# Kernel tuning notes

Measured on AMD Instinct MI355X. Metric: run time of the kernel, lower is better.

Reference implementation:

```python
import jax, jax.numpy as jnp
import numpy as np

N = 50000      # nodes per graph
E = 1600000    # edges per graph
D_IN = 128
D_HID = 128
D_OUT = 128
D_GF = 128
N_LAYERS = 3   # input->hid, hid->hid (hidden_layer=1), hid->out


def setup_inputs() -> dict:
    key = jax.random.key(0)
    ks = jax.random.split(key, 24)
    inp = {
        "feat_p": jax.random.normal(ks[0], (N, D_IN), jnp.float32),
        "src_p": jax.random.randint(ks[1], (E,), 0, N, jnp.int32),
        "dst_p": jax.random.randint(ks[2], (E,), 0, N, jnp.int32),
        "feat_s": jax.random.normal(ks[3], (N, D_IN), jnp.float32),
        "src_s": jax.random.randint(ks[4], (E,), 0, N, jnp.int32),
        "dst_s": jax.random.randint(ks[5], (E,), 0, N, jnp.int32),
    }
    dims = [(D_IN, D_HID), (D_HID, D_HID), (D_HID, D_OUT)]
    for i, (di, do) in enumerate(dims):
        inp[f"W{i}"] = jax.random.normal(ks[6 + 2 * i], (di, do), jnp.float32) * 0.05
        inp[f"b{i}"] = jnp.zeros((do,), jnp.float32)
    inp["Wr"] = jax.random.normal(ks[14], (D_OUT, D_GF), jnp.float32) * 0.05
    inp["br"] = jnp.zeros((D_GF,), jnp.float32)
    inp["Wm1"] = jax.random.normal(ks[15], (2 * D_GF, D_GF), jnp.float32) * 0.05
    inp["bm1"] = jnp.zeros((D_GF,), jnp.float32)
    inp["Wm2"] = jax.random.normal(ks[16], (D_GF, 1), jnp.float32) * 0.05
    inp["bm2"] = jnp.zeros((1,), jnp.float32)
    return inp


def _gcn_stack(feat, src, dst, layers):
    """Stacked GCN: mean over incoming messages, then linear.
    NOTE: the original SingleGCN never applies its ReLU (bug preserved)."""
    n = feat.shape[0]
    deg = jax.ops.segment_sum(jnp.ones_like(src, feat.dtype), dst, num_segments=n)
    inv_deg = (1.0 / jnp.maximum(deg, 1.0))[:, None]  # [N,1]
    h = feat
    for W, b in layers:
        msg = h[src]                                           # [E,d] gather
        agg = jax.ops.segment_sum(msg, dst, num_segments=n)    # [N,d] scatter-add
        h = (agg * inv_deg) @ W + b                            # mean + linear
    return h


def reference(feat_p, src_p, dst_p, feat_s, src_s, dst_s,
              W0, b0, W1, b1, W2, b2, Wr, br, Wm1, bm1, Wm2, bm2):
    layers = [(W0, b0), (W1, b1), (W2, b2)]
    h_p = _gcn_stack(feat_p, src_p, dst_p, layers)
    h_s = _gcn_stack(feat_s, src_s, dst_s, layers)
    # ReadOut: mean over nodes -> linear -> sigmoid
    g_p = jax.nn.sigmoid(jnp.mean(h_p, axis=0) @ Wr + br)  # [D_GF]
    g_s = jax.nn.sigmoid(jnp.mean(h_s, axis=0) @ Wr + br)
    # Match: concat -> linear -> linear -> sigmoid
    c = jnp.concatenate([g_p, g_s], axis=-1)               # [2*D_GF]
    d = (c @ Wm1 + bm1) @ Wm2 + bm2                        # [1]
    return jax.nn.sigmoid(d)
```

## Files before the change

### kernel.cpp

```cpp
#include <hip/hip_runtime.h>
#include <math.h>

#define D 128
#define BSH 9
#define NPB 512
#define BCAP 17920
#define STCAP 6252


__global__ __launch_bounds__(256) void zero_kernel(float* __restrict__ buf, int n4) {
    float4* b4 = (float4*)buf;
    const float4 z = make_float4(0.f, 0.f, 0.f, 0.f);
    const int stride = gridDim.x * 256;
    for (int i = blockIdx.x * 256 + threadIdx.x; i < n4; i += stride) b4[i] = z;
}

__global__ __launch_bounds__(512) void bin_kernel(
        const int* __restrict__ src_p, const int* __restrict__ dst_p,
        const int* __restrict__ src_s, const int* __restrict__ dst_s,
        int* __restrict__ sbins, unsigned short* __restrict__ dbins,
        unsigned* __restrict__ cur, int E, int nbkt) {
    const int g = blockIdx.y;
    const int* src = g ? src_s : src_p;
    const int* dst = g ? dst_s : dst_p;
    int* sb = sbins + (size_t)g * nbkt * BCAP;
    unsigned short* db = dbins + (size_t)g * nbkt * BCAP;
    unsigned* scur = cur + g * nbkt;
    unsigned* dcur = cur + 2 * nbkt + g * nbkt;

    __shared__ int sstage[STCAP];
    __shared__ unsigned short dstage[STCAP];
    __shared__ unsigned hist_s[128], hist_d[128];
    __shared__ unsigned offs_s[128], offs_d[128];
    __shared__ unsigned lcur_s[128], lcur_d[128];
    __shared__ unsigned gb_s[128], gb_d[128];

    const int tid = threadIdx.x;
    const int wv = tid >> 6, lane = tid & 63;
    for (int i = tid; i < 128; i += 512) { hist_s[i] = 0u; hist_d[i] = 0u; }
    __syncthreads();

    const int e0 = blockIdx.x * STCAP;
    const int e1 = min(e0 + STCAP, E);
    const int efull = e0 + ((e1 - e0) & ~3);

    for (int e = e0 + tid * 4; e + 4 <= e1; e += 512 * 4) {
        int4 s4 = *(const int4*)(src + e);
        int4 d4 = *(const int4*)(dst + e);
        atomicAdd(&hist_s[s4.x >> BSH], 1u);
        atomicAdd(&hist_s[s4.y >> BSH], 1u);
        atomicAdd(&hist_s[s4.z >> BSH], 1u);
        atomicAdd(&hist_s[s4.w >> BSH], 1u);
        atomicAdd(&hist_d[d4.x >> BSH], 1u);
        atomicAdd(&hist_d[d4.y >> BSH], 1u);
        atomicAdd(&hist_d[d4.z >> BSH], 1u);
        atomicAdd(&hist_d[d4.w >> BSH], 1u);
    }
    for (int e = efull + tid; e < e1; e += 512) {
        atomicAdd(&hist_s[src[e] >> BSH], 1u);
        atomicAdd(&hist_d[dst[e] >> BSH], 1u);
    }
    __syncthreads();

    if (wv == 0 || wv == 1) {
        const unsigned* h = (wv == 0) ? hist_s : hist_d;
        unsigned* o = (wv == 0) ? offs_s : offs_d;
        unsigned* lc = (wv == 0) ? lcur_s : lcur_d;
        unsigned a = (2 * lane < nbkt) ? h[2 * lane] : 0u;
        unsigned b = (2 * lane + 1 < nbkt) ? h[2 * lane + 1] : 0u;
        unsigned v = a + b;
        for (int d2 = 1; d2 < 64; d2 <<= 1) {
            unsigned t = __shfl_up(v, d2);
            if (lane >= d2) v += t;
        }
        unsigned ex = v - (a + b);
        if (2 * lane < nbkt) { o[2 * lane] = ex; lc[2 * lane] = ex; }
        if (2 * lane + 1 < nbkt) { o[2 * lane + 1] = ex + a; lc[2 * lane + 1] = ex + a; }
    } else if (wv == 2) {
        for (int i = lane; i < nbkt; i += 64) {
            unsigned c = hist_s[i];
            gb_s[i] = c ? atomicAdd(&scur[i], c) : 0u;
        }
    } else if (wv == 3) {
        for (int i = lane; i < nbkt; i += 64) {
            unsigned c = hist_d[i];
            gb_d[i] = c ? atomicAdd(&dcur[i], c) : 0u;
        }
    }
    __syncthreads();

    for (int e = e0 + tid * 4; e + 4 <= e1; e += 512 * 4) {
        int4 s4 = *(const int4*)(src + e);
        int4 d4 = *(const int4*)(dst + e);
        int sv[4] = {s4.x, s4.y, s4.z, s4.w};
        int dv[4] = {d4.x, d4.y, d4.z, d4.w};
        #pragma unroll
        for (int k = 0; k < 4; ++k) {
            unsigned p = atomicAdd(&lcur_s[sv[k] >> BSH], 1u);
            sstage[p] = ((sv[k] & (NPB - 1)) << 17) | dv[k];
            unsigned pd = atomicAdd(&lcur_d[dv[k] >> BSH], 1u);
            dstage[pd] = (unsigned short)(dv[k] & (NPB - 1));
        }
    }
    for (int e = efull + tid; e < e1; e += 512) {
        int s = src[e], d2 = dst[e];
        unsigned p = atomicAdd(&lcur_s[s >> BSH], 1u);
        sstage[p] = ((s & (NPB - 1)) << 17) | d2;
        unsigned pd = atomicAdd(&lcur_d[d2 >> BSH], 1u);
        dstage[pd] = (unsigned short)(d2 & (NPB - 1));
    }
    __syncthreads();

    for (int b = wv; b < nbkt; b += 8) {
        unsigned cs = hist_s[b], os = offs_s[b], gs = gb_s[b];
        unsigned lim = (gs < (unsigned)BCAP) ? min(cs, (unsigned)BCAP - gs) : 0u;
        int* dp = sb + (size_t)b * BCAP + gs;
        for (unsigned i = lane; i < lim; i += 64) dp[i] = sstage[os + i];
        unsigned cd = hist_d[b], od = offs_d[b], gd = gb_d[b];
        unsigned limd = (gd < (unsigned)BCAP) ? min(cd, (unsigned)BCAP - gd) : 0u;
        unsigned short* ddp = db + (size_t)b * BCAP + gd;
        for (unsigned i = lane; i < limd; i += 64) ddp[i] = dstage[od + i];
    }
}

__global__ __launch_bounds__(512) void deg_inv(
        const unsigned short* __restrict__ dbins, const unsigned* __restrict__ cur,
        float* __restrict__ inv, int N, int nbkt) {
    const int q = blockIdx.x, g = blockIdx.y;
    const unsigned short* bin = dbins + (size_t)(g * nbkt + q) * BCAP;
    const int cnt = min((int)cur[2 * nbkt + g * nbkt + q], BCAP);
    const int tid = threadIdx.x;
    const int wv = tid >> 6;
    __shared__ float bl[8][NPB];
    for (int i = tid; i < 8 * NPB; i += 512) ((float*)bl)[i] = 0.f;
    __syncthreads();
    float* mybl = bl[wv];
    const ushort4* b4 = (const ushort4*)bin;
    const int n4 = cnt >> 2;
    for (int i = tid; i < n4; i += 512) {
        ushort4 v = b4[i];
        atomicAdd(&mybl[v.x], 1.f);
        atomicAdd(&mybl[v.y], 1.f);
        atomicAdd(&mybl[v.z], 1.f);
        atomicAdd(&mybl[v.w], 1.f);
    }
    for (int e = (n4 << 2) + tid; e < cnt; e += 512) atomicAdd(&mybl[bin[e]], 1.f);
    __syncthreads();
    float t = 0.f;
    #pragma unroll
    for (int r = 0; r < 8; ++r) t += bl[r][tid];
    int node = q * NPB + tid;
    if (node < N) inv[(size_t)g * N + node] = 1.0f / fmaxf(t, 1.0f);
}

__global__ __launch_bounds__(512) void prop_scan(
        const int* __restrict__ sbins, const unsigned* __restrict__ cur,
        const float* __restrict__ w, const float* __restrict__ inv,
        float* __restrict__ out_w, float* __restrict__ out_u,
        float* __restrict__ sums, int s_idx, int N, int nbkt, float scale) {
    const int q = blockIdx.x, g = blockIdx.y;
    const int* bin = sbins + (size_t)(g * nbkt + q) * BCAP;
    const int cnt = min((int)cur[g * nbkt + q], BCAP);
    const float* wg = w + (size_t)g * N;
    const int tid = threadIdx.x;
    const int wv = tid >> 6;
    __shared__ float bl[8][NPB];
    __shared__ float red[512];
    for (int i = tid; i < 8 * NPB; i += 512) ((float*)bl)[i] = 0.f;
    __syncthreads();
    float* mybl = bl[wv];
    const int4* b4 = (const int4*)bin;
    const int n4 = cnt >> 2;
    for (int i = tid; i < n4; i += 512) {
        int4 v = b4[i];
        float a = wg[v.x & 0x1FFFF];
        float b = wg[v.y & 0x1FFFF];
        float c = wg[v.z & 0x1FFFF];
        float d2 = wg[v.w & 0x1FFFF];
        atomicAdd(&mybl[((unsigned)v.x) >> 17], a);
        atomicAdd(&mybl[((unsigned)v.y) >> 17], b);
        atomicAdd(&mybl[((unsigned)v.z) >> 17], c);
        atomicAdd(&mybl[((unsigned)v.w) >> 17], d2);
    }
    for (int e = (n4 << 2) + tid; e < cnt; e += 512) {
        int v = bin[e];
        atomicAdd(&mybl[((unsigned)v) >> 17], wg[v & 0x1FFFF]);
    }
    __syncthreads();
    float t = 0.f;
    #pragma unroll
    for (int r = 0; r < 8; ++r) t += bl[r][tid];
    const float u = t * scale;
    const int node = q * NPB + tid;
    const bool valid = node < N;
    if (valid) {
        size_t off = (size_t)g * N + node;
        if (out_w) out_w[off] = u * inv[off];
        if (out_u) out_u[off] = u;
    }
    if (sums) {
        red[tid] = valid ? u : 0.f;
        __syncthreads();
        for (int st = 256; st > 0; st >>= 1) {
            if (tid < st) red[tid] += red[tid + st];
            __syncthreads();
        }
        if (tid == 0 && red[0] != 0.f) atomicAdd(&sums[g * 2 + s_idx], red[0]);
    }
}

__global__ __launch_bounds__(256) void featsum_kernel(
        const float* __restrict__ feat_p, const float* __restrict__ feat_s,
        const float* __restrict__ u3, float* __restrict__ fpart2,
        int N, int rpb) {
    const int g = blockIdx.y;
    const float* feat = g ? feat_s : feat_p;
    const float* u = u3 + (size_t)g * N;
    const int col4 = threadIdx.x & 31;
    const int rgrp = threadIdx.x >> 5;
    const int r0 = blockIdx.x * rpb;
    const int r1 = min(r0 + rpb, N);

    const float4* f4 = (const float4*)feat;
    float4 acc = make_float4(0.f, 0.f, 0.f, 0.f);
    for (int n = r0 + rgrp * 4; n + 3 < r1; n += 32) {
        float4 uu = *(const float4*)(u + n);
        float4 v0 = f4[(size_t)n * 32 + col4];
        float4 v1 = f4[(size_t)(n + 1) * 32 + col4];
        float4 v2 = f4[(size_t)(n + 2) * 32 + col4];
        float4 v3 = f4[(size_t)(n + 3) * 32 + col4];
        acc.x += uu.x * v0.x + uu.y * v1.x + uu.z * v2.x + uu.w * v3.x;
        acc.y += uu.x * v0.y + uu.y * v1.y + uu.z * v2.y + uu.w * v3.y;
        acc.z += uu.x * v0.z + uu.y * v1.z + uu.z * v2.z + uu.w * v3.z;
        acc.w += uu.x * v0.w + uu.y * v1.w + uu.z * v2.w + uu.w * v3.w;
    }
    __shared__ float4 smem[256];
    smem[threadIdx.x] = acc;
    __syncthreads();
    if (rgrp == 0) {
        float4 t = smem[col4];
        #pragma unroll
        for (int k = 1; k < 8; k++) {
            float4 o = smem[k * 32 + col4];
            t.x += o.x; t.y += o.y; t.z += o.z; t.w += o.w;
        }
        float* dst = fpart2 + ((size_t)g * 16 + (blockIdx.x & 15)) * 128 + col4 * 4;
        atomicAdd(dst + 0, t.x);
        atomicAdd(dst + 1, t.y);
        atomicAdd(dst + 2, t.z);
        atomicAdd(dst + 3, t.w);
    }
}

__global__ __launch_bounds__(512) void final_kernel(
        const float* __restrict__ fpart2,
        const float* __restrict__ sums,
        const float* __restrict__ W0, const float* __restrict__ b0,
        const float* __restrict__ W1, const float* __restrict__ b1,
        const float* __restrict__ W2, const float* __restrict__ b2,
        const float* __restrict__ Wr, const float* __restrict__ br,
        const float* __restrict__ Wm1, const float* __restrict__ bm1,
        const float* __restrict__ Wm2, const float* __restrict__ bm2,
        float* __restrict__ out) {
    __shared__ float x[128];
    __shared__ float part[4][128];
    __shared__ float rvec[256];
    __shared__ float Avec[128], Bvec[128];
    __shared__ float gv[256];
    const int tid = threadIdx.x;
    const int j = tid & 127;
    const int h = tid >> 7;

    auto mv128 = [&](const float* __restrict__ W, float* __restrict__ buf) {
        float p = 0.f;
        const float* Wp = W + (size_t)(h * 32) * 128 + j;
        #pragma unroll
        for (int i = 0; i < 32; ++i) p += buf[h * 32 + i] * Wp[(size_t)i * 128];
        part[h][j] = p;
        __syncthreads();
        if (h == 0) buf[j] = part[0][j] + part[1][j] + part[2][j] + part[3][j];
        __syncthreads();
    };

    if (tid < 256) {
        int g = tid >> 7;
        const float* fp = fpart2 + (size_t)g * 2048 + (tid & 127);
        float rv = 0.f;
        #pragma unroll
        for (int b = 0; b < 16; ++b) rv += fp[(size_t)b * 128];
        rvec[tid] = rv;
    }
    __syncthreads();

    if (tid < 128) x[tid] = b0[tid];
    __syncthreads();
    mv128(W1, x);
    mv128(W2, x);
    if (tid < 128) Avec[tid] = x[tid];
    __syncthreads();
    if (tid < 128) x[tid] = b1[tid];
    __syncthreads();
    mv128(W2, x);
    if (tid < 128) Bvec[tid] = x[tid];
    __syncthreads();

    for (int g = 0; g < 2; ++g) {
        const float s1 = sums[g * 2 + 0];
        const float s2 = sums[g * 2 + 1];
        if (tid < 128) x[tid] = rvec[g * 128 + tid];
        __syncthreads();
        mv128(W0, x);
        mv128(W1, x);
        mv128(W2, x);
        if (tid < 128) x[tid] += s2 * Avec[tid] + s1 * Bvec[tid] + b2[tid];
        __syncthreads();
        mv128(Wr, x);
        if (tid < 128) gv[g * 128 + tid] = 1.0f / (1.0f + expf(-(x[tid] + br[tid])));
        __syncthreads();
    }

    {
        float p = 0.f;
        const float* Wp = Wm1 + (size_t)(h * 64) * 128 + j;
        #pragma unroll
        for (int i = 0; i < 64; ++i) p += gv[h * 64 + i] * Wp[(size_t)i * 128];
        part[h][j] = p;
        __syncthreads();
        if (h == 0)
            part[0][j] = (part[0][j] + part[1][j] + part[2][j] + part[3][j] + bm1[j]) * Wm2[j];
        __syncthreads();
        if (tid < 64) part[0][tid] += part[0][tid + 64];
        __syncthreads();
        if (tid < 32) part[0][tid] += part[0][tid + 32];
        __syncthreads();
        if (tid < 16) part[0][tid] += part[0][tid + 16];
        __syncthreads();
        if (tid < 8) part[0][tid] += part[0][tid + 8];
        __syncthreads();
        if (tid < 4) part[0][tid] += part[0][tid + 4];
        __syncthreads();
        if (tid < 2) part[0][tid] += part[0][tid + 2];
        __syncthreads();
        if (tid == 0) out[0] = 1.0f / (1.0f + expf(-(part[0][0] + part[0][1] + bm2[0])));
    }
}

extern "C" void kernel_launch(void* const* d_in, const int* in_sizes, int n_in,
                              void* d_out, int out_size, void* d_ws, size_t ws_size,
                              hipStream_t stream) {
    const float* feat_p = (const float*)d_in[0];
    const int*   src_p  = (const int*)d_in[1];
    const int*   dst_p  = (const int*)d_in[2];
    const float* feat_s = (const float*)d_in[3];
    const int*   src_s  = (const int*)d_in[4];
    const int*   dst_s  = (const int*)d_in[5];
    const float* W0 = (const float*)d_in[6];
    const float* b0 = (const float*)d_in[7];
    const float* W1 = (const float*)d_in[8];
    const float* b1 = (const float*)d_in[9];
    const float* W2 = (const float*)d_in[10];
    const float* b2 = (const float*)d_in[11];
    const float* Wr = (const float*)d_in[12];
    const float* br = (const float*)d_in[13];
    const float* Wm1 = (const float*)d_in[14];
    const float* bm1 = (const float*)d_in[15];
    const float* Wm2 = (const float*)d_in[16];
    const float* bm2 = (const float*)d_in[17];
    float* out = (float*)d_out;

    const int N = in_sizes[0] / D;
    const int E = in_sizes[1];
    const int N2 = 2 * N;
    const int nbkt = (N + NPB - 1) >> BSH;
    const int NBB = (E + STCAP - 1) / STCAP;
    const int FB = 256;
    const int rpb = (((N + FB - 1) / FB) + 3) & ~3;

    float* ws       = (float*)d_ws;
    unsigned* cur   = (unsigned*)ws;
    const int curN  = (4 * nbkt + 3) & ~3;
    float* sums     = ws + curN;
    float* fpart2   = sums + 16;
    float* inv      = fpart2 + 2 * 16 * 128;
    float* w1       = inv + N2;
    float* w2       = w1 + N2;
    float* u3       = w2 + N2;
    int*   sbins    = (int*)(u3 + N2);
    unsigned short* dbins = (unsigned short*)(sbins + (size_t)2 * nbkt * BCAP);

    const float u0 = 1.0f / (float)N;
    const int zc4 = (curN + 16 + 2 * 16 * 128) / 4;

    zero_kernel<<<16, 256, 0, stream>>>(ws, zc4);

    bin_kernel<<<dim3(NBB, 2), 512, 0, stream>>>(src_p, dst_p, src_s, dst_s,
                                                 sbins, dbins, cur, E, nbkt);

    deg_inv<<<dim3(nbkt, 2), 512, 0, stream>>>(dbins, cur, inv, N, nbkt);

    prop_scan<<<dim3(nbkt, 2), 512, 0, stream>>>(sbins, cur, inv, inv,
                                                 w1, nullptr, sums, 0,
                                                 N, nbkt, u0);
    prop_scan<<<dim3(nbkt, 2), 512, 0, stream>>>(sbins, cur, w1, inv,
                                                 w2, nullptr, sums, 1,
                                                 N, nbkt, 1.0f);
    prop_scan<<<dim3(nbkt, 2), 512, 0, stream>>>(sbins, cur, w2, inv,
                                                 nullptr, u3, nullptr, 0,
                                                 N, nbkt, 1.0f);

    featsum_kernel<<<dim3(FB, 2), 256, 0, stream>>>(feat_p, feat_s, u3, fpart2, N, rpb);

    final_kernel<<<1, 512, 0, stream>>>(fpart2, sums, W0, b0, W1, b1, W2, b2,
                                        Wr, br, Wm1, bm1, Wm2, bm2, out);
}
```

Measured before the change: 279.4 us.

## Use fixed per-block bin slots, drop global atomics, fuse featsum into last propagation

The binning kernel now writes each edge block's bucket contents into a fixed-size per-(bucket, block) slot with a count array. This replaces global atomic cursors into shared bins, so the zero kernel goes away and the workspace is instead cleared inside deg_inv. The feature-weighted node sum is folded into the final propagation pass, which removes the separate featsum kernel and the u3 buffer. In exchange, readers now scan padded slots with per-element bounds checks. Any block-bucket holding more than 128 edges is silently truncated, and the zeroing inside deg_inv must finish before the later kernels read sums and fpart2.

```diff
diff --git a/kernel.cpp b/kernel.cpp
--- a/kernel.cpp
+++ b/kernel.cpp
@@ -4,43 +4,38 @@
 #define D 128
 #define BSH 9
 #define NPB 512
-#define BCAP 17920
+#define SLOT 128
 #define STCAP 6252
-
-
-__global__ __launch_bounds__(256) void zero_kernel(float* __restrict__ buf, int n4) {
-    float4* b4 = (float4*)buf;
-    const float4 z = make_float4(0.f, 0.f, 0.f, 0.f);
-    const int stride = gridDim.x * 256;
-    for (int i = blockIdx.x * 256 + threadIdx.x; i < n4; i += stride) b4[i] = z;
-}
+#define NBB 256
+#define NBKT_MAX 128
+
 
 __global__ __launch_bounds__(512) void bin_kernel(
         const int* __restrict__ src_p, const int* __restrict__ dst_p,
         const int* __restrict__ src_s, const int* __restrict__ dst_s,
         int* __restrict__ sbins, unsigned short* __restrict__ dbins,
-        unsigned* __restrict__ cur, int E, int nbkt) {
-    const int g = blockIdx.y;
+        unsigned* __restrict__ cnt_s, unsigned* __restrict__ cnt_d,
+        int E, int nbkt) {
+    const int g = blockIdx.y, b = blockIdx.x;
     const int* src = g ? src_s : src_p;
     const int* dst = g ? dst_s : dst_p;
-    int* sb = sbins + (size_t)g * nbkt * BCAP;
-    unsigned short* db = dbins + (size_t)g * nbkt * BCAP;
-    unsigned* scur = cur + g * nbkt;
-    unsigned* dcur = cur + 2 * nbkt + g * nbkt;
+    int* sb = sbins + (size_t)g * nbkt * NBB * SLOT;
+    unsigned short* db = dbins + (size_t)g * nbkt * NBB * SLOT;
+    unsigned* csp = cnt_s + (size_t)g * nbkt * NBB;
+    unsigned* cdp = cnt_d + (size_t)g * nbkt * NBB;
 
     __shared__ int sstage[STCAP];
     __shared__ unsigned short dstage[STCAP];
-    __shared__ unsigned hist_s[128], hist_d[128];
-    __shared__ unsigned offs_s[128], offs_d[128];
-    __shared__ unsigned lcur_s[128], lcur_d[128];
-    __shared__ unsigned gb_s[128], gb_d[128];
+    __shared__ unsigned hist_s[NBKT_MAX], hist_d[NBKT_MAX];
+    __shared__ unsigned offs_s[NBKT_MAX], offs_d[NBKT_MAX];
+    __shared__ unsigned lcur_s[NBKT_MAX], lcur_d[NBKT_MAX];
 
     const int tid = threadIdx.x;
     const int wv = tid >> 6, lane = tid & 63;
-    for (int i = tid; i < 128; i += 512) { hist_s[i] = 0u; hist_d[i] = 0u; }
-    __syncthreads();
-
-    const int e0 = blockIdx.x * STCAP;
+    for (int i = tid; i < NBKT_MAX; i += 512) { hist_s[i] = 0u; hist_d[i] = 0u; }
+    __syncthreads();
+
+    const int e0 = b * STCAP;
     const int e1 = min(e0 + STCAP, E);
     const int efull = e0 + ((e1 - e0) & ~3);
 
@@ -67,25 +62,15 @@
         unsigned* o = (wv == 0) ? offs_s : offs_d;
         unsigned* lc = (wv == 0) ? lcur_s : lcur_d;
         unsigned a = (2 * lane < nbkt) ? h[2 * lane] : 0u;
-        unsigned b = (2 * lane + 1 < nbkt) ? h[2 * lane + 1] : 0u;
-        unsigned v = a + b;
+        unsigned bb = (2 * lane + 1 < nbkt) ? h[2 * lane + 1] : 0u;
+        unsigned v = a + bb;
         for (int d2 = 1; d2 < 64; d2 <<= 1) {
             unsigned t = __shfl_up(v, d2);
             if (lane >= d2) v += t;
         }
-        unsigned ex = v - (a + b);
+        unsigned ex = v - (a + bb);
         if (2 * lane < nbkt) { o[2 * lane] = ex; lc[2 * lane] = ex; }
         if (2 * lane + 1 < nbkt) { o[2 * lane + 1] = ex + a; lc[2 * lane + 1] = ex + a; }
-    } else if (wv == 2) {
-        for (int i = lane; i < nbkt; i += 64) {
-            unsigned c = hist_s[i];
-            gb_s[i] = c ? atomicAdd(&scur[i], c) : 0u;
-        }
-    } else if (wv == 3) {
-        for (int i = lane; i < nbkt; i += 64) {
-            unsigned c = hist_d[i];
-            gb_d[i] = c ? atomicAdd(&dcur[i], c) : 0u;
-        }
     }
     __syncthreads();
 
@@ -111,40 +96,45 @@
     }
     __syncthreads();
 
-    for (int b = wv; b < nbkt; b += 8) {
-        unsigned cs = hist_s[b], os = offs_s[b], gs = gb_s[b];
-        unsigned lim = (gs < (unsigned)BCAP) ? min(cs, (unsigned)BCAP - gs) : 0u;
-        int* dp = sb + (size_t)b * BCAP + gs;
-        for (unsigned i = lane; i < lim; i += 64) dp[i] = sstage[os + i];
-        unsigned cd = hist_d[b], od = offs_d[b], gd = gb_d[b];
-        unsigned limd = (gd < (unsigned)BCAP) ? min(cd, (unsigned)BCAP - gd) : 0u;
-        unsigned short* ddp = db + (size_t)b * BCAP + gd;
-        for (unsigned i = lane; i < limd; i += 64) ddp[i] = dstage[od + i];
+    for (int q = wv; q < nbkt; q += 8) {
+        unsigned cs = min(hist_s[q], (unsigned)SLOT);
+        unsigned os = offs_s[q];
+        int* dp = sb + ((size_t)q * NBB + b) * SLOT;
+        for (unsigned i = lane; i < cs; i += 64) dp[i] = sstage[os + i];
+        unsigned cd = min(hist_d[q], (unsigned)SLOT);
+        unsigned od = offs_d[q];
+        unsigned short* ddp = db + ((size_t)q * NBB + b) * SLOT;
+        for (unsigned i = lane; i < cd; i += 64) ddp[i] = dstage[od + i];
+        if (lane == 0) { csp[q * NBB + b] = cs; cdp[q * NBB + b] = cd; }
     }
 }
 
 __global__ __launch_bounds__(512) void deg_inv(
-        const unsigned short* __restrict__ dbins, const unsigned* __restrict__ cur,
-        float* __restrict__ inv, int N, int nbkt) {
+        const unsigned short* __restrict__ dbins, const unsigned* __restrict__ cnt_d,
+        float* __restrict__ inv, float* __restrict__ zbase, int zcount,
+        int N, int nbkt) {
     const int q = blockIdx.x, g = blockIdx.y;
-    const unsigned short* bin = dbins + (size_t)(g * nbkt + q) * BCAP;
-    const int cnt = min((int)cur[2 * nbkt + g * nbkt + q], BCAP);
-    const int tid = threadIdx.x;
-    const int wv = tid >> 6;
+    const int tid = threadIdx.x, wv = tid >> 6;
+    if (q == 0 && g == 0)
+        for (int i = tid; i < zcount; i += 512) zbase[i] = 0.f;
+    const unsigned short* dq = dbins + ((size_t)g * nbkt + q) * NBB * SLOT;
+    const unsigned* cq = cnt_d + (size_t)g * nbkt * NBB + (size_t)q * NBB;
     __shared__ float bl[8][NPB];
+    __shared__ unsigned lcnt[NBB];
+    if (tid < NBB) lcnt[tid] = cq[tid];
     for (int i = tid; i < 8 * NPB; i += 512) ((float*)bl)[i] = 0.f;
     __syncthreads();
     float* mybl = bl[wv];
-    const ushort4* b4 = (const ushort4*)bin;
-    const int n4 = cnt >> 2;
-    for (int i = tid; i < n4; i += 512) {
-        ushort4 v = b4[i];
+    const ushort4* d4 = (const ushort4*)dq;
+    for (int i = tid; i < NBB * (SLOT / 4); i += 512) {
+        int lim = (int)lcnt[i >> 5] - ((i & 31) << 2);
+        if (lim <= 0) continue;
+        ushort4 v = d4[i];
         atomicAdd(&mybl[v.x], 1.f);
-        atomicAdd(&mybl[v.y], 1.f);
-        atomicAdd(&mybl[v.z], 1.f);
-        atomicAdd(&mybl[v.w], 1.f);
-    }
-    for (int e = (n4 << 2) + tid; e < cnt; e += 512) atomicAdd(&mybl[bin[e]], 1.f);
+        if (lim > 1) atomicAdd(&mybl[v.y], 1.f);
+        if (lim > 2) atomicAdd(&mybl[v.z], 1.f);
+        if (lim > 3) atomicAdd(&mybl[v.w], 1.f);
+    }
     __syncthreads();
     float t = 0.f;
     #pragma unroll
@@ -154,37 +144,40 @@
 }
 
 __global__ __launch_bounds__(512) void prop_scan(
-        const int* __restrict__ sbins, const unsigned* __restrict__ cur,
+        const int* __restrict__ sbins, const unsigned* __restrict__ cnt_s,
         const float* __restrict__ w, const float* __restrict__ inv,
-        float* __restrict__ out_w, float* __restrict__ out_u,
-        float* __restrict__ sums, int s_idx, int N, int nbkt, float scale) {
+        float* __restrict__ out_w,
+        const float* __restrict__ feat_p, const float* __restrict__ feat_s,
+        float* __restrict__ fpart2, float* __restrict__ sums, int s_idx,
+        int N, int nbkt, float scale) {
     const int q = blockIdx.x, g = blockIdx.y;
-    const int* bin = sbins + (size_t)(g * nbkt + q) * BCAP;
-    const int cnt = min((int)cur[g * nbkt + q], BCAP);
+    const int* sq = sbins + ((size_t)g * nbkt + q) * NBB * SLOT;
+    const unsigned* cq = cnt_s + (size_t)g * nbkt * NBB + (size_t)q * NBB;
     const float* wg = w + (size_t)g * N;
-    const int tid = threadIdx.x;
-    const int wv = tid >> 6;
+    const int tid = threadIdx.x, wv = tid >> 6;
     __shared__ float bl[8][NPB];
-    __shared__ float red[512];
+    __shared__ unsigned lcnt[NBB];
+    __shared__ float red[NPB];
+    if (tid < NBB) lcnt[tid] = cq[tid];
     for (int i = tid; i < 8 * NPB; i += 512) ((float*)bl)[i] = 0.f;
     __syncthreads();
     float* mybl = bl[wv];
-    const int4* b4 = (const int4*)bin;
-    const int n4 = cnt >> 2;
-    for (int i = tid; i < n4; i += 512) {
-        int4 v = b4[i];
+    const int4* s4 = (const int4*)sq;
+    for (int i = tid; i < NBB * (SLOT / 4); i += 512) {
+        int lim = (int)lcnt[i >> 5] - ((i & 31) << 2);
+        if (lim <= 0) continue;
+        int4 v = s4[i];
+        int iy = (lim > 1) ? (v.y & 0x1FFFF) : 0;
+        int iz = (lim > 2) ? (v.z & 0x1FFFF) : 0;
+        int iw = (lim > 3) ? (v.w & 0x1FFFF) : 0;
         float a = wg[v.x & 0x1FFFF];
-        float b = wg[v.y & 0x1FFFF];
-        float c = wg[v.z & 0x1FFFF];
-        float d2 = wg[v.w & 0x1FFFF];
+        float b2 = wg[iy];
+        float c2 = wg[iz];
+        float d2 = wg[iw];
         atomicAdd(&mybl[((unsigned)v.x) >> 17], a);
-        atomicAdd(&mybl[((unsigned)v.y) >> 17], b);
-        atomicAdd(&mybl[((unsigned)v.z) >> 17], c);
-        atomicAdd(&mybl[((unsigned)v.w) >> 17], d2);
-    }
-    for (int e = (n4 << 2) + tid; e < cnt; e += 512) {
-        int v = bin[e];
-        atomicAdd(&mybl[((unsigned)v) >> 17], wg[v & 0x1FFFF]);
+        if (lim > 1) atomicAdd(&mybl[((unsigned)v.y) >> 17], b2);
+        if (lim > 2) atomicAdd(&mybl[((unsigned)v.z) >> 17], c2);
+        if (lim > 3) atomicAdd(&mybl[((unsigned)v.w) >> 17], d2);
     }
     __syncthreads();
     float t = 0.f;
@@ -193,10 +186,9 @@
     const float u = t * scale;
     const int node = q * NPB + tid;
     const bool valid = node < N;
-    if (valid) {
+    if (valid && out_w) {
         size_t off = (size_t)g * N + node;
-        if (out_w) out_w[off] = u * inv[off];
-        if (out_u) out_u[off] = u;
+        out_w[off] = u * inv[off];
     }
     if (sums) {
         red[tid] = valid ? u : 0.f;
@@ -207,48 +199,24 @@
         }
         if (tid == 0 && red[0] != 0.f) atomicAdd(&sums[g * 2 + s_idx], red[0]);
     }
-}
-
-__global__ __launch_bounds__(256) void featsum_kernel(
-        const float* __restrict__ feat_p, const float* __restrict__ feat_s,
-        const float* __restrict__ u3, float* __restrict__ fpart2,
-        int N, int rpb) {
-    const int g = blockIdx.y;
-    const float* feat = g ? feat_s : feat_p;
-    const float* u = u3 + (size_t)g * N;
-    const int col4 = threadIdx.x & 31;
-    const int rgrp = threadIdx.x >> 5;
-    const int r0 = blockIdx.x * rpb;
-    const int r1 = min(r0 + rpb, N);
-
-    const float4* f4 = (const float4*)feat;
-    float4 acc = make_float4(0.f, 0.f, 0.f, 0.f);
-    for (int n = r0 + rgrp * 4; n + 3 < r1; n += 32) {
-        float4 uu = *(const float4*)(u + n);
-        float4 v0 = f4[(size_t)n * 32 + col4];
-        float4 v1 = f4[(size_t)(n + 1) * 32 + col4];
-        float4 v2 = f4[(size_t)(n + 2) * 32 + col4];
-        float4 v3 = f4[(size_t)(n + 3) * 32 + col4];
-        acc.x += uu.x * v0.x + uu.y * v1.x + uu.z * v2.x + uu.w * v3.x;
-        acc.y += uu.x * v0.y + uu.y * v1.y + uu.z * v2.y + uu.w * v3.y;
-        acc.z += uu.x * v0.z + uu.y * v1.z + uu.z * v2.z + uu.w * v3.z;
-        acc.w += uu.x * v0.w + uu.y * v1.w + uu.z * v2.w + uu.w * v3.w;
-    }
-    __shared__ float4 smem[256];
-    smem[threadIdx.x] = acc;
-    __syncthreads();
-    if (rgrp == 0) {
-        float4 t = smem[col4];
-        #pragma unroll
-        for (int k = 1; k < 8; k++) {
-            float4 o = smem[k * 32 + col4];
-            t.x += o.x; t.y += o.y; t.z += o.z; t.w += o.w;
+    if (fpart2) {
+        red[tid] = valid ? u : 0.f;
+        __syncthreads();
+        const float* feat = g ? feat_s : feat_p;
+        const int j = tid & 127, rg = tid >> 7;
+        const int base = q * NPB;
+        const int rmax = min(NPB, N - base);
+        float acc = 0.f;
+        const int rend = min((rg + 1) * 128, rmax);
+        for (int r = rg * 128; r < rend; ++r)
+            acc += red[r] * feat[(size_t)(base + r) * D + j];
+        ((float*)bl)[rg * 128 + j] = acc;
+        __syncthreads();
+        if (rg == 0) {
+            float tot = ((float*)bl)[j] + ((float*)bl)[128 + j] +
+                        ((float*)bl)[256 + j] + ((float*)bl)[384 + j];
+            atomicAdd(&fpart2[((size_t)g * 16 + (q & 15)) * D + j], tot);
         }
-        float* dst = fpart2 + ((size_t)g * 16 + (blockIdx.x & 15)) * 128 + col4 * 4;
-        atomicAdd(dst + 0, t.x);
-        atomicAdd(dst + 1, t.y);
-        atomicAdd(dst + 2, t.z);
-        atomicAdd(dst + 3, t.w);
     }
 }
 
@@ -372,43 +340,37 @@
     const int E = in_sizes[1];
     const int N2 = 2 * N;
     const int nbkt = (N + NPB - 1) >> BSH;
-    const int NBB = (E + STCAP - 1) / STCAP;
-    const int FB = 256;
-    const int rpb = (((N + FB - 1) / FB) + 3) & ~3;
-
-    float* ws       = (float*)d_ws;
-    unsigned* cur   = (unsigned*)ws;
-    const int curN  = (4 * nbkt + 3) & ~3;
-    float* sums     = ws + curN;
-    float* fpart2   = sums + 16;
-    float* inv      = fpart2 + 2 * 16 * 128;
-    float* w1       = inv + N2;
-    float* w2       = w1 + N2;
-    float* u3       = w2 + N2;
-    int*   sbins    = (int*)(u3 + N2);
-    unsigned short* dbins = (unsigned short*)(sbins + (size_t)2 * nbkt * BCAP);
+
+    float* ws     = (float*)d_ws;
+    float* sums   = ws;
+    float* fpart2 = ws + 16;
+    float* inv    = fpart2 + 2 * 16 * 128;
+    float* w1     = inv + N2;
+    float* w2     = w1 + N2;
+    unsigned* cnt_s = (unsigned*)(w2 + N2);
+    unsigned* cnt_d = cnt_s + (size_t)2 * nbkt * NBB;
+    int* sbins    = (int*)(cnt_d + (size_t)2 * nbkt * NBB);
+    unsigned short* dbins = (unsigned short*)(sbins + (size_t)2 * nbkt * NBB * SLOT);
 
     const float u0 = 1.0f / (float)N;
-    const int zc4 = (curN + 16 + 2 * 16 * 128) / 4;
-
-    zero_kernel<<<16, 256, 0, stream>>>(ws, zc4);
+    const int zcount = 16 + 2 * 16 * 128;
 
     bin_kernel<<<dim3(NBB, 2), 512, 0, stream>>>(src_p, dst_p, src_s, dst_s,
-                                                 sbins, dbins, cur, E, nbkt);
-
-    deg_inv<<<dim3(nbkt, 2), 512, 0, stream>>>(dbins, cur, inv, N, nbkt);
-
-    prop_scan<<<dim3(nbkt, 2), 512, 0, stream>>>(sbins, cur, inv, inv,
-                                                 w1, nullptr, sums, 0,
-                                                 N, nbkt, u0);
-    prop_scan<<<dim3(nbkt, 2), 512, 0, stream>>>(sbins, cur, w1, inv,
-                                                 w2, nullptr, sums, 1,
-                                                 N, nbkt, 1.0f);
-    prop_scan<<<dim3(nbkt, 2), 512, 0, stream>>>(sbins, cur, w2, inv,
-                                                 nullptr, u3, nullptr, 0,
-                                                 N, nbkt, 1.0f);
-
-    featsum_kernel<<<dim3(FB, 2), 256, 0, stream>>>(feat_p, feat_s, u3, fpart2, N, rpb);
+                                                 sbins, dbins, cnt_s, cnt_d,
+                                                 E, nbkt);
+
+    deg_inv<<<dim3(nbkt, 2), 512, 0, stream>>>(dbins, cnt_d, inv, ws, zcount,
+                                               N, nbkt);
+
+    prop_scan<<<dim3(nbkt, 2), 512, 0, stream>>>(sbins, cnt_s, inv, inv, w1,
+                                                 nullptr, nullptr, nullptr,
+                                                 sums, 0, N, nbkt, u0);
+    prop_scan<<<dim3(nbkt, 2), 512, 0, stream>>>(sbins, cnt_s, w1, inv, w2,
+                                                 nullptr, nullptr, nullptr,
+                                                 sums, 1, N, nbkt, 1.0f);
+    prop_scan<<<dim3(nbkt, 2), 512, 0, stream>>>(sbins, cnt_s, w2, inv, nullptr,
+                                                 feat_p, feat_s, fpart2,
+                                                 nullptr, 0, N, nbkt, 1.0f);
 
     final_kernel<<<1, 512, 0, stream>>>(fpart2, sums, W0, b0, W1, b1, W2, b2,
                                         Wr, br, Wm1, bm1, Wm2, bm2, out);
```

New measurement: 317.2 us. +13.5%, slower.
